# Optimization experiments

Measured on AMD Instinct MI355X. Metric: run time of the kernel, lower is better.

The kernel has to match this reference:

```python
import jax, jax.numpy as jnp
import numpy as np
import math

N_HEADS = 8
FACTOR = 1


def setup_inputs() -> dict:
    key = jax.random.key(0)
    k1, k2, k3 = jax.random.split(key, 3)
    B, L, E = 16, 2048, 512
    return {
        "queries": jax.random.normal(k1, (B, L, E), dtype=jnp.float32),
        "keys": jax.random.normal(k2, (B, L, E), dtype=jnp.float32),
        "values": jax.random.normal(k3, (B, L, E), dtype=jnp.float32),
        "attn_mask": jnp.zeros((1,), dtype=bool),  # unused by the original forward
    }


def _time_delay_agg(values, corr, factor):
    # values, corr: (B, H, L, C)
    B, H, L, C = values.shape
    top_k = max(1, int(factor * math.log(L)))
    # NOTE: topk over the last (channel) axis, faithfully matching the source.
    weights, delay = jax.lax.top_k(corr, top_k)          # (B,H,L,K)
    weights = jax.nn.softmax(weights, axis=-1)
    positions = jnp.arange(L).reshape(1, 1, L, 1)
    delay_idx = (positions - delay) % L                   # (B,H,L,K), time indices
    idx = delay_idx.reshape(B, H, L * top_k, 1)
    gathered = jnp.take_along_axis(values, idx, axis=2)   # (B,H,L*K,C)
    gathered = gathered.reshape(B, H, L, top_k, C)
    return (gathered * weights[..., None]).sum(axis=3)    # (B,H,L,C)


def reference(queries, keys, values, attn_mask):
    B, L, E = queries.shape
    _, S, _ = values.shape
    H = N_HEADS
    hd = E // H
    q = queries.reshape(B, L, H, hd).transpose(0, 2, 1, 3)  # (B,H,L,hd)
    k = keys.reshape(B, S, H, hd).transpose(0, 2, 1, 3)
    v = values.reshape(B, S, H, hd).transpose(0, 2, 1, 3)
    if L > S:
        pad = L - S
        zeros = jnp.zeros((B, H, pad, hd), dtype=v.dtype)
        v = jnp.concatenate([v, zeros], axis=2)
        k = jnp.concatenate([k, zeros], axis=2)
    else:
        v = v[:, :, :L, :]
        k = k[:, :, :L, :]
    # period-based dependency discovery via FFT cross-correlation along time
    q_fft = jnp.fft.rfft(q, axis=2)
    k_fft = jnp.fft.rfft(k, axis=2)
    corr = jnp.fft.irfft(q_fft * jnp.conj(k_fft), n=L, axis=2)  # (B,H,L,hd)
    out = _time_delay_agg(v, corr, FACTOR)                       # (B,H,L,hd)
    return out.transpose(0, 2, 1, 3).reshape(B, L, E)
```

## Files before the change

### kernel.cpp

```cpp
#include <hip/hip_runtime.h>
#include <math.h>

#define LEN   2048
#define EDIM  512
#define NB    16
#define NH    8
#define HD    64
#define TOPK  7
#define LBLK  128
#define VROWS (LBLK + 64)

__device__ inline float2 cmul(float2 a, float2 b) {
    return make_float2(a.x * b.x - a.y * b.y, a.x * b.y + a.y * b.x);
}
__device__ inline float2 cadd(float2 a, float2 b) { return make_float2(a.x + b.x, a.y + b.y); }
__device__ inline float2 csub(float2 a, float2 b) { return make_float2(a.x - b.x, a.y - b.y); }
__device__ inline int sw(int i) { return i ^ ((i >> 5) & 15); }

__global__ __launch_bounds__(256) void transpose_qk(const float* __restrict__ q,
                                                    const float* __restrict__ k,
                                                    float* __restrict__ qT,
                                                    float* __restrict__ kT) {
    __shared__ float tile[64][65];
    int b  = blockIdx.z;
    int e0 = blockIdx.x * 64;
    int t0 = blockIdx.y * 64;
    int tid = threadIdx.x;
    int tr = tid >> 4, cx = tid & 15;
    int er = tid >> 2, tg = tid & 3;
    const float* qb = q + (size_t)b * LEN * EDIM;
    const float* kb = k + (size_t)b * LEN * EDIM;
    float* qTb = qT + (size_t)b * EDIM * LEN;
    float* kTb = kT + (size_t)b * EDIM * LEN;

    #pragma unroll
    for (int i = 0; i < 4; ++i) {
        int row = tr + 16 * i;
        float4 v = *(const float4*)(qb + (size_t)(t0 + row) * EDIM + e0 + 4 * cx);
        tile[4 * cx + 0][row] = v.x;
        tile[4 * cx + 1][row] = v.y;
        tile[4 * cx + 2][row] = v.z;
        tile[4 * cx + 3][row] = v.w;
    }
    __syncthreads();
    #pragma unroll
    for (int i = 0; i < 4; ++i) {
        int seg = tg + 4 * i;
        float4 v = make_float4(tile[er][4 * seg + 0], tile[er][4 * seg + 1],
                               tile[er][4 * seg + 2], tile[er][4 * seg + 3]);
        *(float4*)(qTb + (size_t)(e0 + er) * LEN + t0 + 4 * seg) = v;
    }
    __syncthreads();
    #pragma unroll
    for (int i = 0; i < 4; ++i) {
        int row = tr + 16 * i;
        float4 v = *(const float4*)(kb + (size_t)(t0 + row) * EDIM + e0 + 4 * cx);
        tile[4 * cx + 0][row] = v.x;
        tile[4 * cx + 1][row] = v.y;
        tile[4 * cx + 2][row] = v.z;
        tile[4 * cx + 3][row] = v.w;
    }
    __syncthreads();
    #pragma unroll
    for (int i = 0; i < 4; ++i) {
        int seg = tg + 4 * i;
        float4 v = make_float4(tile[er][4 * seg + 0], tile[er][4 * seg + 1],
                               tile[er][4 * seg + 2], tile[er][4 * seg + 3]);
        *(float4*)(kTb + (size_t)(e0 + er) * LEN + t0 + 4 * seg) = v;
    }
}

__device__ inline void tw8(float ang, float2* w) {
    float s, c;
    sincosf(ang, &s, &c);
    w[1] = make_float2(c, s);
    w[2] = cmul(w[1], w[1]);
    w[3] = cmul(w[2], w[1]);
    w[4] = cmul(w[2], w[2]);
    w[5] = cmul(w[3], w[2]);
    w[6] = cmul(w[3], w[3]);
    w[7] = cmul(w[4], w[3]);
}

__device__ inline void fwd8(float2* P, int base, int stride, const float2* w) {
    const float C = 0.70710678118654752f;
    float2 v[8];
    #pragma unroll
    for (int r = 0; r < 8; ++r) v[r] = P[sw(base + stride * r)];
    float2 y0 = cadd(v[0], v[4]), y1 = cadd(v[1], v[5]);
    float2 y2 = cadd(v[2], v[6]), y3 = cadd(v[3], v[7]);
    float2 t0 = csub(v[0], v[4]), t1 = csub(v[1], v[5]);
    float2 t2 = csub(v[2], v[6]), t3 = csub(v[3], v[7]);
    float2 z0 = t0;
    float2 z1 = make_float2(C * (t1.x + t1.y), C * (t1.y - t1.x));
    float2 z2 = make_float2(t2.y, -t2.x);
    float2 z3 = make_float2(C * (t3.y - t3.x), -C * (t3.x + t3.y));
    float2 a0 = cadd(y0, y2), a1 = cadd(y1, y3);
    float2 b0 = csub(y0, y2), tb = csub(y1, y3);
    float2 b1 = make_float2(tb.y, -tb.x);
    float2 c0 = cadd(z0, z2), c1 = cadd(z1, z3);
    float2 d0 = csub(z0, z2), td = csub(z1, z3);
    float2 d1 = make_float2(td.y, -td.x);
    float2 X0 = cadd(a0, a1), X4 = csub(a0, a1);
    float2 X2 = cadd(b0, b1), X6 = csub(b0, b1);
    float2 X1 = cadd(c0, c1), X5 = csub(c0, c1);
    float2 X3 = cadd(d0, d1), X7 = csub(d0, d1);
    P[sw(base)]              = X0;
    P[sw(base + stride)]     = cmul(X1, w[1]);
    P[sw(base + 2 * stride)] = cmul(X2, w[2]);
    P[sw(base + 3 * stride)] = cmul(X3, w[3]);
    P[sw(base + 4 * stride)] = cmul(X4, w[4]);
    P[sw(base + 5 * stride)] = cmul(X5, w[5]);
    P[sw(base + 6 * stride)] = cmul(X6, w[6]);
    P[sw(base + 7 * stride)] = cmul(X7, w[7]);
}

__device__ inline void inv8(float2* P, int base, int stride, const float2* w) {
    const float C = 0.70710678118654752f;
    float2 v[8];
    #pragma unroll
    for (int p = 0; p < 8; ++p) v[p] = P[sw(base + stride * p)];
    #pragma unroll
    for (int p = 1; p < 8; ++p) v[p] = cmul(v[p], w[p]);
    float2 y0 = cadd(v[0], v[4]), y1 = cadd(v[1], v[5]);
    float2 y2 = cadd(v[2], v[6]), y3 = cadd(v[3], v[7]);
    float2 t0 = csub(v[0], v[4]), t1 = csub(v[1], v[5]);
    float2 t2 = csub(v[2], v[6]), t3 = csub(v[3], v[7]);
    float2 z0 = t0;
    float2 z1 = make_float2(C * (t1.x - t1.y), C * (t1.x + t1.y));
    float2 z2 = make_float2(-t2.y, t2.x);
    float2 z3 = make_float2(-C * (t3.x + t3.y), C * (t3.x - t3.y));
    float2 a0 = cadd(y0, y2), a1 = cadd(y1, y3);
    float2 b0 = csub(y0, y2), tb = csub(y1, y3);
    float2 b1 = make_float2(-tb.y, tb.x);
    float2 c0 = cadd(z0, z2), c1 = cadd(z1, z3);
    float2 d0 = csub(z0, z2), td = csub(z1, z3);
    float2 d1 = make_float2(-td.y, td.x);
    float2 X0 = cadd(a0, a1), X4 = csub(a0, a1);
    float2 X2 = cadd(b0, b1), X6 = csub(b0, b1);
    float2 X1 = cadd(c0, c1), X5 = csub(c0, c1);
    float2 X3 = cadd(d0, d1), X7 = csub(d0, d1);
    P[sw(base)]              = X0;
    P[sw(base + stride)]     = X1;
    P[sw(base + 2 * stride)] = X2;
    P[sw(base + 3 * stride)] = X3;
    P[sw(base + 4 * stride)] = X4;
    P[sw(base + 5 * stride)] = X5;
    P[sw(base + 6 * stride)] = X6;
    P[sw(base + 7 * stride)] = X7;
}

__device__ inline void fwd4(float2* P, int base) {
    float2 v0 = P[sw(base)], v1 = P[sw(base + 1)], v2 = P[sw(base + 2)], v3 = P[sw(base + 3)];
    float2 a0 = cadd(v0, v2), a1 = cadd(v1, v3);
    float2 b0 = csub(v0, v2), t = csub(v1, v3);
    float2 b1 = make_float2(t.y, -t.x);
    P[sw(base)]     = cadd(a0, a1);
    P[sw(base + 2)] = csub(a0, a1);
    P[sw(base + 1)] = cadd(b0, b1);
    P[sw(base + 3)] = csub(b0, b1);
}
__device__ inline void inv4(float2* P, int base) {
    float2 v0 = P[sw(base)], v1 = P[sw(base + 1)], v2 = P[sw(base + 2)], v3 = P[sw(base + 3)];
    float2 a0 = cadd(v0, v2), a1 = cadd(v1, v3);
    float2 b0 = csub(v0, v2), t = csub(v1, v3);
    float2 b1 = make_float2(-t.y, t.x);
    P[sw(base)]     = cadd(a0, a1);
    P[sw(base + 2)] = csub(a0, a1);
    P[sw(base + 1)] = cadd(b0, b1);
    P[sw(base + 3)] = csub(b0, b1);
}

__device__ inline int slotOf(int k) {
    return ((k & 7) << 8) | (((k >> 3) & 7) << 5) | (((k >> 6) & 7) << 2) | ((k >> 9) & 3);
}

__device__ inline void fft_core(float2* A, float2* Bs, int tid) {
    const float PI2 = 6.283185307179586f;
    float2 w[8];
    tw8(-PI2 * (float)tid * (1.0f / 2048.0f), w);
    fwd8(A, tid, 256, w);
    fwd8(Bs, tid, 256, w);
    __syncthreads();
    {
        int c = tid >> 5, q = tid & 31, base = c * 256 + q;
        tw8(-PI2 * (float)q * (1.0f / 256.0f), w);
        fwd8(A, base, 32, w);
        fwd8(Bs, base, 32, w);
    }
    __syncthreads();
    {
        int c = tid >> 2, q = tid & 3, base = c * 32 + q;
        tw8(-PI2 * (float)q * (1.0f / 32.0f), w);
        fwd8(A, base, 4, w);
        fwd8(Bs, base, 4, w);
    }
    __syncthreads();
    fwd4(A, 4 * tid);  fwd4(A, 4 * (tid + 256));
    fwd4(Bs, 4 * tid); fwd4(Bs, 4 * (tid + 256));
    __syncthreads();
    for (int f = tid; f <= 1024; f += 256) {
        int nf = (2048 - f) & 2047;
        int ia = sw(slotOf(f));
        int ib = sw(slotOf(nf));
        float2 z1 = A[ia],  z1n = A[ib];
        float2 z2 = Bs[ia], z2n = Bs[ib];
        float Qx = 0.5f * (z1.x + z1n.x), Qy = 0.5f * (z1.y - z1n.y);
        float Kx = 0.5f * (z1.y + z1n.y), Ky = 0.5f * (z1n.x - z1.x);
        float C1x = Qx * Kx + Qy * Ky;
        float C1y = Qy * Kx - Qx * Ky;
        float Px = 0.5f * (z2.x + z2n.x), Py = 0.5f * (z2.y - z2n.y);
        float Lx = 0.5f * (z2.y + z2n.y), Ly = 0.5f * (z2n.x - z2.x);
        float C2x = Px * Lx + Py * Ly;
        float C2y = Py * Lx - Px * Ly;
        A[ia] = make_float2(C1x - C2y, C1y + C2x);
        if (f != 0 && f != 1024)
            A[ib] = make_float2(C1x + C2y, C2x - C1y);
    }
    __syncthreads();
    inv4(A, 4 * tid); inv4(A, 4 * (tid + 256));
    __syncthreads();
    {
        int c = tid >> 2, q = tid & 3, base = c * 32 + q;
        tw8(PI2 * (float)q * (1.0f / 32.0f), w);
        inv8(A, base, 4, w);
    }
    __syncthreads();
    {
        int c = tid >> 5, q = tid & 31, base = c * 256 + q;
        tw8(PI2 * (float)q * (1.0f / 256.0f), w);
        inv8(A, base, 32, w);
    }
    __syncthreads();
    tw8(PI2 * (float)tid * (1.0f / 2048.0f), w);
    inv8(A, tid, 256, w);
    __syncthreads();
}

__global__ __launch_bounds__(256, 5) void fft_corr(const float* qT,
                                                   const float* kT,
                                                   float* corr) {
    __shared__ float2 A[LEN];
    __shared__ float2 Bs[LEN];
    int ch0 = blockIdx.x * 2;
    int tid = threadIdx.x;
    const float4* q4 = (const float4*)(qT + (size_t)ch0 * LEN);
    const float4* k4 = (const float4*)(kT + (size_t)ch0 * LEN);
    for (int t4 = tid; t4 < LEN / 4; t4 += 256) {
        float4 qa = q4[t4],           ka = k4[t4];
        float4 qb = q4[t4 + LEN / 4], kb = k4[t4 + LEN / 4];
        int t = t4 * 4;
        A[sw(t)]      = make_float2(qa.x, ka.x);
        A[sw(t + 1)]  = make_float2(qa.y, ka.y);
        A[sw(t + 2)]  = make_float2(qa.z, ka.z);
        A[sw(t + 3)]  = make_float2(qa.w, ka.w);
        Bs[sw(t)]     = make_float2(qb.x, kb.x);
        Bs[sw(t + 1)] = make_float2(qb.y, kb.y);
        Bs[sw(t + 2)] = make_float2(qb.z, kb.z);
        Bs[sw(t + 3)] = make_float2(qb.w, kb.w);
    }
    __syncthreads();
    fft_core(A, Bs, tid);
    const float inv = 1.0f / (float)LEN;
    float4* c0 = (float4*)(corr + (size_t)ch0 * LEN);
    float4* c1 = (float4*)(corr + (size_t)(ch0 + 1) * LEN);
    for (int t4 = tid; t4 < LEN / 4; t4 += 256) {
        int t = t4 * 4;
        float2 e0 = A[sw(t)], e1 = A[sw(t + 1)], e2 = A[sw(t + 2)], e3 = A[sw(t + 3)];
        c0[t4] = make_float4(e0.x * inv, e1.x * inv, e2.x * inv, e3.x * inv);
        c1[t4] = make_float4(e0.y * inv, e1.y * inv, e2.y * inv, e3.y * inv);
    }
}

__global__ __launch_bounds__(256, 5) void fft_corr_strided(const float* q,
                                                           const float* k,
                                                           float* corr,
                                                           int chStart) {
    __shared__ float2 A[LEN];
    __shared__ float2 Bs[LEN];
    int chLocal = blockIdx.x * 2;
    int gch = chStart + chLocal;
    int b   = gch >> 9;
    int e   = gch & (EDIM - 1);
    int tid = threadIdx.x;
    const float* qr = q + (size_t)b * LEN * EDIM + e;
    const float* kr = k + (size_t)b * LEN * EDIM + e;
    for (int t = tid; t < LEN; t += 256) {
        float2 qv = *(const float2*)(qr + (size_t)t * EDIM);
        float2 kv = *(const float2*)(kr + (size_t)t * EDIM);
        A[sw(t)]  = make_float2(qv.x, kv.x);
        Bs[sw(t)] = make_float2(qv.y, kv.y);
    }
    __syncthreads();
    fft_core(A, Bs, tid);
    const float inv = 1.0f / (float)LEN;
    float4* c0 = (float4*)(corr + (size_t)chLocal * LEN);
    float4* c1 = (float4*)(corr + (size_t)(chLocal + 1) * LEN);
    for (int t4 = tid; t4 < LEN / 4; t4 += 256) {
        int t = t4 * 4;
        float2 e0 = A[sw(t)], e1 = A[sw(t + 1)], e2 = A[sw(t + 2)], e3 = A[sw(t + 3)];
        c0[t4] = make_float4(e0.x * inv, e1.x * inv, e2.x * inv, e3.x * inv);
        c1[t4] = make_float4(e0.y * inv, e1.y * inv, e2.y * inv, e3.y * inv);
    }
}

__global__ __launch_bounds__(256, 2) void topk_agg(const float* __restrict__ corr,
                                                   const float* __restrict__ values,
                                                   float* __restrict__ out,
                                                   int bhBase) {
    __shared__ float  vtile[VROWS][HD];
    __shared__ float2 w_d[LBLK][TOPK];
    int l0 = blockIdx.x * LBLK;
    int lh = blockIdx.y;
    int bh = bhBase + lh;
    int b  = bh >> 3;
    int h  = bh & 7;
    int tid = threadIdx.x;
    const float* vb0 = values + (size_t)b * LEN * EDIM + h * HD;

    for (int idx = tid; idx < VROWS * (HD / 4); idx += 256) {
        int r  = idx >> 4;
        int c4 = idx & 15;
        int gr = (l0 - 64 + r) & (LEN - 1);
        float4 v = *(const float4*)(vb0 + (size_t)gr * EDIM + 4 * c4);
        *(float4*)&vtile[r][4 * c4] = v;
    }

    if (tid < LBLK) {
        const float* cb = corr + (size_t)lh * HD * LEN + l0 + tid;
        float wk[TOPK];
        int   dk[TOPK];
        #pragma unroll
        for (int t = 0; t < TOPK; ++t) { wk[t] = -INFINITY; dk[t] = 0; }
        #pragma unroll 8
        for (int c = 0; c < HD; ++c) {
            float nv = cb[(size_t)c * LEN];
            int   nd = c;
            #pragma unroll
            for (int t = 0; t < TOPK; ++t) {
                bool  m  = nv > wk[t];
                float tv = wk[t]; int td = dk[t];
                wk[t] = m ? nv : tv;
                dk[t] = m ? nd : td;
                nv    = m ? tv : nv;
                nd    = m ? td : nd;
            }
        }
        float mx = wk[0], sum = 0.f;
        float e[TOPK];
        #pragma unroll
        for (int t = 0; t < TOPK; ++t) { e[t] = expf(wk[t] - mx); sum += e[t]; }
        float invs = 1.f / sum;
        #pragma unroll
        for (int t = 0; t < TOPK; ++t)
            w_d[tid][t] = make_float2(e[t] * invs, __int_as_float(dk[t]));
    }
    __syncthreads();

    int lane = tid & 63;
    int wave = tid >> 6;
    float* ob = out + (size_t)b * LEN * EDIM + h * HD + lane;
    for (int i = 0; i < LBLK / 4; ++i) {
        int lp = wave * (LBLK / 4) + i;
        int l  = l0 + lp;
        float acc = 0.f;
        #pragma unroll
        for (int t = 0; t < TOPK; ++t) {
            float2 wd = w_d[lp][t];
            int r = lp - __float_as_int(wd.y) + 64;
            acc += wd.x * vtile[r][lane];
        }
        ob[(size_t)l * EDIM] = acc;
    }
}

extern "C" void kernel_launch(void* const* d_in, const int* in_sizes, int n_in,
                              void* d_out, int out_size, void* d_ws, size_t ws_size,
                              hipStream_t stream) {
    const float* q = (const float*)d_in[0];
    const float* k = (const float*)d_in[1];
    const float* v = (const float*)d_in[2];
    float* out = (float*)d_out;

    const size_t CORR_BYTES = (size_t)NB * EDIM * LEN * sizeof(float);

    if (ws_size >= CORR_BYTES) {
        float* qT   = (float*)d_ws;
        float* kT   = (float*)d_out;
        float* corr = qT;
        transpose_qk<<<dim3(EDIM / 64, LEN / 64, NB), dim3(256), 0, stream>>>(q, k, qT, kT);
        fft_corr<<<dim3(NB * EDIM / 2), dim3(256), 0, stream>>>(qT, kT, corr);
        topk_agg<<<dim3(LEN / LBLK, NB * NH), dim3(256), 0, stream>>>(corr, v, out, 0);
    } else {
        const size_t HEAD_BYTES = (size_t)HD * LEN * sizeof(float);
        int headsPer = (int)(ws_size / HEAD_BYTES);
        if (headsPer < 1) headsPer = 1;
        if (headsPer > NB * NH) headsPer = NB * NH;
        float* corr = (float*)d_ws;
        for (int hs = 0; hs < NB * NH; hs += headsPer) {
            int hc = NB * NH - hs < headsPer ? NB * NH - hs : headsPer;
            fft_corr_strided<<<dim3(hc * HD / 2), dim3(256), 0, stream>>>(q, k, corr, hs * HD);
            topk_agg<<<dim3(LEN / LBLK, hc), dim3(256), 0, stream>>>(corr, v, out, hs);
        }
    }
}
```

Measured before the change: 369.7 us.

## Drop transpose kernel, read strided inputs directly and gather values from global

Removes the separate transpose pass so the FFT correlation kernel reads q and k straight from the (B,L,E) layout with strided float2 loads, eliminating one full write and read of the transposed tensors. The top-k/aggregation kernel now uses 256 positions per block with every thread doing top-k, and gathers value rows directly from global memory instead of staging a shared-memory tile. Occupancy hints are removed. The strided loads are poorly coalesced (8 bytes per 2KB row stride) and the value gathers rely on cache hits, so effective bandwidth may drop.

```diff
diff --git a/kernel.cpp b/kernel.cpp
--- a/kernel.cpp
+++ b/kernel.cpp
@@ -7,8 +7,6 @@
 #define NH    8
 #define HD    64
 #define TOPK  7
-#define LBLK  128
-#define VROWS (LBLK + 64)
 
 __device__ inline float2 cmul(float2 a, float2 b) {
     return make_float2(a.x * b.x - a.y * b.y, a.x * b.y + a.y * b.x);
@@ -16,59 +14,6 @@
 __device__ inline float2 cadd(float2 a, float2 b) { return make_float2(a.x + b.x, a.y + b.y); }
 __device__ inline float2 csub(float2 a, float2 b) { return make_float2(a.x - b.x, a.y - b.y); }
 __device__ inline int sw(int i) { return i ^ ((i >> 5) & 15); }
-
-__global__ __launch_bounds__(256) void transpose_qk(const float* __restrict__ q,
-                                                    const float* __restrict__ k,
-                                                    float* __restrict__ qT,
-                                                    float* __restrict__ kT) {
-    __shared__ float tile[64][65];
-    int b  = blockIdx.z;
-    int e0 = blockIdx.x * 64;
-    int t0 = blockIdx.y * 64;
-    int tid = threadIdx.x;
-    int tr = tid >> 4, cx = tid & 15;
-    int er = tid >> 2, tg = tid & 3;
-    const float* qb = q + (size_t)b * LEN * EDIM;
-    const float* kb = k + (size_t)b * LEN * EDIM;
-    float* qTb = qT + (size_t)b * EDIM * LEN;
-    float* kTb = kT + (size_t)b * EDIM * LEN;
-
-    #pragma unroll
-    for (int i = 0; i < 4; ++i) {
-        int row = tr + 16 * i;
-        float4 v = *(const float4*)(qb + (size_t)(t0 + row) * EDIM + e0 + 4 * cx);
-        tile[4 * cx + 0][row] = v.x;
-        tile[4 * cx + 1][row] = v.y;
-        tile[4 * cx + 2][row] = v.z;
-        tile[4 * cx + 3][row] = v.w;
-    }
-    __syncthreads();
-    #pragma unroll
-    for (int i = 0; i < 4; ++i) {
-        int seg = tg + 4 * i;
-        float4 v = make_float4(tile[er][4 * seg + 0], tile[er][4 * seg + 1],
-                               tile[er][4 * seg + 2], tile[er][4 * seg + 3]);
-        *(float4*)(qTb + (size_t)(e0 + er) * LEN + t0 + 4 * seg) = v;
-    }
-    __syncthreads();
-    #pragma unroll
-    for (int i = 0; i < 4; ++i) {
-        int row = tr + 16 * i;
-        float4 v = *(const float4*)(kb + (size_t)(t0 + row) * EDIM + e0 + 4 * cx);
-        tile[4 * cx + 0][row] = v.x;
-        tile[4 * cx + 1][row] = v.y;
-        tile[4 * cx + 2][row] = v.z;
-        tile[4 * cx + 3][row] = v.w;
-    }
-    __syncthreads();
-    #pragma unroll
-    for (int i = 0; i < 4; ++i) {
-        int seg = tg + 4 * i;
-        float4 v = make_float4(tile[er][4 * seg + 0], tile[er][4 * seg + 1],
-                               tile[er][4 * seg + 2], tile[er][4 * seg + 3]);
-        *(float4*)(kTb + (size_t)(e0 + er) * LEN + t0 + 4 * seg) = v;
-    }
-}
 
 __device__ inline void tw8(float ang, float2* w) {
     float s, c;
@@ -237,45 +182,10 @@
     __syncthreads();
 }
 
-__global__ __launch_bounds__(256, 5) void fft_corr(const float* qT,
-                                                   const float* kT,
-                                                   float* corr) {
-    __shared__ float2 A[LEN];
-    __shared__ float2 Bs[LEN];
-    int ch0 = blockIdx.x * 2;
-    int tid = threadIdx.x;
-    const float4* q4 = (const float4*)(qT + (size_t)ch0 * LEN);
-    const float4* k4 = (const float4*)(kT + (size_t)ch0 * LEN);
-    for (int t4 = tid; t4 < LEN / 4; t4 += 256) {
-        float4 qa = q4[t4],           ka = k4[t4];
-        float4 qb = q4[t4 + LEN / 4], kb = k4[t4 + LEN / 4];
-        int t = t4 * 4;
-        A[sw(t)]      = make_float2(qa.x, ka.x);
-        A[sw(t + 1)]  = make_float2(qa.y, ka.y);
-        A[sw(t + 2)]  = make_float2(qa.z, ka.z);
-        A[sw(t + 3)]  = make_float2(qa.w, ka.w);
-        Bs[sw(t)]     = make_float2(qb.x, kb.x);
-        Bs[sw(t + 1)] = make_float2(qb.y, kb.y);
-        Bs[sw(t + 2)] = make_float2(qb.z, kb.z);
-        Bs[sw(t + 3)] = make_float2(qb.w, kb.w);
-    }
-    __syncthreads();
-    fft_core(A, Bs, tid);
-    const float inv = 1.0f / (float)LEN;
-    float4* c0 = (float4*)(corr + (size_t)ch0 * LEN);
-    float4* c1 = (float4*)(corr + (size_t)(ch0 + 1) * LEN);
-    for (int t4 = tid; t4 < LEN / 4; t4 += 256) {
-        int t = t4 * 4;
-        float2 e0 = A[sw(t)], e1 = A[sw(t + 1)], e2 = A[sw(t + 2)], e3 = A[sw(t + 3)];
-        c0[t4] = make_float4(e0.x * inv, e1.x * inv, e2.x * inv, e3.x * inv);
-        c1[t4] = make_float4(e0.y * inv, e1.y * inv, e2.y * inv, e3.y * inv);
-    }
-}
-
-__global__ __launch_bounds__(256, 5) void fft_corr_strided(const float* q,
-                                                           const float* k,
-                                                           float* corr,
-                                                           int chStart) {
+__global__ __launch_bounds__(256) void fft_corr_strided(const float* __restrict__ q,
+                                                        const float* __restrict__ k,
+                                                        float* __restrict__ corr,
+                                                        int chStart) {
     __shared__ float2 A[LEN];
     __shared__ float2 Bs[LEN];
     int chLocal = blockIdx.x * 2;
@@ -285,7 +195,9 @@
     int tid = threadIdx.x;
     const float* qr = q + (size_t)b * LEN * EDIM + e;
     const float* kr = k + (size_t)b * LEN * EDIM + e;
-    for (int t = tid; t < LEN; t += 256) {
+    #pragma unroll
+    for (int j = 0; j < LEN / 256; ++j) {
+        int t = tid + 256 * j;
         float2 qv = *(const float2*)(qr + (size_t)t * EDIM);
         float2 kv = *(const float2*)(kr + (size_t)t * EDIM);
         A[sw(t)]  = make_float2(qv.x, kv.x);
@@ -304,71 +216,60 @@
     }
 }
 
-__global__ __launch_bounds__(256, 2) void topk_agg(const float* __restrict__ corr,
-                                                   const float* __restrict__ values,
-                                                   float* __restrict__ out,
-                                                   int bhBase) {
-    __shared__ float  vtile[VROWS][HD];
-    __shared__ float2 w_d[LBLK][TOPK];
-    int l0 = blockIdx.x * LBLK;
+__global__ __launch_bounds__(256) void topk_agg(const float* __restrict__ corr,
+                                                const float* __restrict__ values,
+                                                float* __restrict__ out,
+                                                int bhBase) {
+    __shared__ float2 w_d[256][TOPK];
+    int l0 = blockIdx.x * 256;
     int lh = blockIdx.y;
     int bh = bhBase + lh;
     int b  = bh >> 3;
     int h  = bh & 7;
     int tid = threadIdx.x;
-    const float* vb0 = values + (size_t)b * LEN * EDIM + h * HD;
-
-    for (int idx = tid; idx < VROWS * (HD / 4); idx += 256) {
-        int r  = idx >> 4;
-        int c4 = idx & 15;
-        int gr = (l0 - 64 + r) & (LEN - 1);
-        float4 v = *(const float4*)(vb0 + (size_t)gr * EDIM + 4 * c4);
-        *(float4*)&vtile[r][4 * c4] = v;
-    }
-
-    if (tid < LBLK) {
-        const float* cb = corr + (size_t)lh * HD * LEN + l0 + tid;
-        float wk[TOPK];
-        int   dk[TOPK];
+
+    const float* cb = corr + (size_t)lh * HD * LEN + l0 + tid;
+    float wk[TOPK];
+    int   dk[TOPK];
+    #pragma unroll
+    for (int t = 0; t < TOPK; ++t) { wk[t] = -INFINITY; dk[t] = 0; }
+    #pragma unroll 8
+    for (int c = 0; c < HD; ++c) {
+        float nv = cb[(size_t)c * LEN];
+        int   nd = c;
         #pragma unroll
-        for (int t = 0; t < TOPK; ++t) { wk[t] = -INFINITY; dk[t] = 0; }
-        #pragma unroll 8
-        for (int c = 0; c < HD; ++c) {
-            float nv = cb[(size_t)c * LEN];
-            int   nd = c;
-            #pragma unroll
-            for (int t = 0; t < TOPK; ++t) {
-                bool  m  = nv > wk[t];
-                float tv = wk[t]; int td = dk[t];
-                wk[t] = m ? nv : tv;
-                dk[t] = m ? nd : td;
-                nv    = m ? tv : nv;
-                nd    = m ? td : nd;
-            }
+        for (int t = 0; t < TOPK; ++t) {
+            bool  m  = nv > wk[t];
+            float tv = wk[t]; int td = dk[t];
+            wk[t] = m ? nv : tv;
+            dk[t] = m ? nd : td;
+            nv    = m ? tv : nv;
+            nd    = m ? td : nd;
         }
-        float mx = wk[0], sum = 0.f;
-        float e[TOPK];
-        #pragma unroll
-        for (int t = 0; t < TOPK; ++t) { e[t] = expf(wk[t] - mx); sum += e[t]; }
-        float invs = 1.f / sum;
-        #pragma unroll
-        for (int t = 0; t < TOPK; ++t)
-            w_d[tid][t] = make_float2(e[t] * invs, __int_as_float(dk[t]));
-    }
+    }
+    float mx = wk[0], sum = 0.f;
+    float e[TOPK];
+    #pragma unroll
+    for (int t = 0; t < TOPK; ++t) { e[t] = expf(wk[t] - mx); sum += e[t]; }
+    float invs = 1.f / sum;
+    #pragma unroll
+    for (int t = 0; t < TOPK; ++t)
+        w_d[tid][t] = make_float2(e[t] * invs, __int_as_float(dk[t]));
     __syncthreads();
 
     int lane = tid & 63;
     int wave = tid >> 6;
-    float* ob = out + (size_t)b * LEN * EDIM + h * HD + lane;
-    for (int i = 0; i < LBLK / 4; ++i) {
-        int lp = wave * (LBLK / 4) + i;
+    const float* vb = values + (size_t)b * LEN * EDIM + h * HD + lane;
+    float*       ob = out    + (size_t)b * LEN * EDIM + h * HD + lane;
+    for (int i = 0; i < 64; ++i) {
+        int lp = wave * 64 + i;
         int l  = l0 + lp;
         float acc = 0.f;
         #pragma unroll
         for (int t = 0; t < TOPK; ++t) {
             float2 wd = w_d[lp][t];
-            int r = lp - __float_as_int(wd.y) + 64;
-            acc += wd.x * vtile[r][lane];
+            int idx = (l - __float_as_int(wd.y)) & (LEN - 1);
+            acc += wd.x * vb[(size_t)idx * EDIM];
         }
         ob[(size_t)l * EDIM] = acc;
     }
@@ -385,12 +286,9 @@
     const size_t CORR_BYTES = (size_t)NB * EDIM * LEN * sizeof(float);
 
     if (ws_size >= CORR_BYTES) {
-        float* qT   = (float*)d_ws;
-        float* kT   = (float*)d_out;
-        float* corr = qT;
-        transpose_qk<<<dim3(EDIM / 64, LEN / 64, NB), dim3(256), 0, stream>>>(q, k, qT, kT);
-        fft_corr<<<dim3(NB * EDIM / 2), dim3(256), 0, stream>>>(qT, kT, corr);
-        topk_agg<<<dim3(LEN / LBLK, NB * NH), dim3(256), 0, stream>>>(corr, v, out, 0);
+        float* corr = (float*)d_ws;
+        fft_corr_strided<<<dim3(NB * EDIM / 2), dim3(256), 0, stream>>>(q, k, corr, 0);
+        topk_agg<<<dim3(LEN / 256, NB * NH), dim3(256), 0, stream>>>(corr, v, out, 0);
     } else {
         const size_t HEAD_BYTES = (size_t)HD * LEN * sizeof(float);
         int headsPer = (int)(ws_size / HEAD_BYTES);
@@ -400,7 +298,7 @@
         for (int hs = 0; hs < NB * NH; hs += headsPer) {
             int hc = NB * NH - hs < headsPer ? NB * NH - hs : headsPer;
             fft_corr_strided<<<dim3(hc * HD / 2), dim3(256), 0, stream>>>(q, k, corr, hs * HD);
-            topk_agg<<<dim3(LEN / LBLK, hc), dim3(256), 0, stream>>>(corr, v, out, hs);
+            topk_agg<<<dim3(LEN / 256, hc), dim3(256), 0, stream>>>(corr, v, out, hs);
         }
     }
 }
```

Result: slower. 431.9 us (+16.8%).
